# Kernel tuning notes

Hardware: AMD Instinct MI355X
Metric: run time of the kernel (lower is better)

## Reference

```python
import jax, jax.numpy as jnp
import numpy as np

N = 50000
HEADS1, HIM = 8, 16
NEG_SLOPE = 0.2


def gat_conv(x, src, dst, W, a_src, a_dst, bias, heads, out_dim, concat):
    n = x.shape[0]
    h = (x @ W).reshape(n, heads, out_dim)                      # [N,H,D]
    al_src = jnp.einsum('nhd,hd->nh', h, a_src)                  # [N,H]
    al_dst = jnp.einsum('nhd,hd->nh', h, a_dst)                  # [N,H]
    e = jax.nn.leaky_relu(al_src[src] + al_dst[dst], NEG_SLOPE)  # [E,H]
    # segment softmax over incoming edges of each destination node
    e_max = jax.ops.segment_max(e, dst, num_segments=n)
    e_max = jnp.where(jnp.isfinite(e_max), e_max, 0.0)
    ex = jnp.exp(e - e_max[dst])
    denom = jax.ops.segment_sum(ex, dst, num_segments=n)
    denom = jnp.where(denom == 0.0, 1.0, denom)
    alpha = ex / denom[dst]                                      # [E,H]
    msg = h[src] * alpha[:, :, None]                             # [E,H,D]
    out = jax.ops.segment_sum(msg, dst, num_segments=n)          # [N,H,D]
    out = out.reshape(n, heads * out_dim) if concat else out.mean(axis=1)
    return out + bias


def setup_inputs() -> dict:
    key = jax.random.key(0)
    ks = jax.random.split(key, 12)
    num_feature, out_feature, him = 128, 121, HIM
    E = 800000
    x = jax.random.normal(ks[0], (N, num_feature), dtype=jnp.float32)
    edge_index = jax.random.randint(ks[1], (2, E), 0, N, dtype=jnp.int64)
    s = 0.1
    W1 = jax.random.normal(ks[2], (num_feature, HEADS1 * him), dtype=jnp.float32) * s
    a_src1 = jax.random.normal(ks[3], (HEADS1, him), dtype=jnp.float32) * s
    a_dst1 = jax.random.normal(ks[4], (HEADS1, him), dtype=jnp.float32) * s
    b1 = jnp.zeros((HEADS1 * him,), dtype=jnp.float32)
    W2 = jax.random.normal(ks[5], (HEADS1 * him, out_feature), dtype=jnp.float32) * s
    a_src2 = jax.random.normal(ks[6], (1, out_feature), dtype=jnp.float32) * s
    a_dst2 = jax.random.normal(ks[7], (1, out_feature), dtype=jnp.float32) * s
    b2 = jnp.zeros((out_feature,), dtype=jnp.float32)
    return {"x": x, "edge_index": edge_index, "W1": W1, "a_src1": a_src1,
            "a_dst1": a_dst1, "b1": b1, "W2": W2, "a_src2": a_src2,
            "a_dst2": a_dst2, "b2": b2}


def reference(x, edge_index, W1, a_src1, a_dst1, b1, W2, a_src2, a_dst2, b2):
    n = x.shape[0]
    loops = jnp.arange(n, dtype=edge_index.dtype)
    src = jnp.concatenate([edge_index[0], loops])  # add self-loops (PyG default)
    dst = jnp.concatenate([edge_index[1], loops])
    h = gat_conv(x, src, dst, W1, a_src1, a_dst1, b1, HEADS1, HIM, True)
    h = jax.nn.relu(h)
    out = gat_conv(h, src, dst, W2, a_src2, a_dst2, b2, 1, W2.shape[1], True)
    return out
```

## Files before the change

### kernel.cpp

```cpp
#include <hip/hip_runtime.h>
#include <hip/hip_fp16.h>

#define NEG_SLOPE 0.2f

typedef __fp16 half8v __attribute__((ext_vector_type(8)));
typedef float f32x4 __attribute__((ext_vector_type(4)));
typedef unsigned uint4u __attribute__((ext_vector_type(4), aligned(4)));
typedef float f32x4u __attribute__((ext_vector_type(4), aligned(4)));

__device__ __forceinline__ float lrelu(float x) {
    return fmaxf(x, 0.0f) + NEG_SLOPE * fminf(x, 0.0f);
}

__device__ __forceinline__ unsigned fkey(float f) {
    unsigned u = __float_as_uint(f);
    return (u & 0x80000000u) ? ~u : (u | 0x80000000u);
}
__device__ __forceinline__ float funkey(unsigned k) {
    return __uint_as_float((k & 0x80000000u) ? (k & 0x7fffffffu) : ~k);
}


__global__ void pack_kernel(const int* __restrict__ src, const int* __restrict__ dst,
                            unsigned* __restrict__ kv, int E) {
    int e = blockIdx.x * 256 + threadIdx.x;
    if (e < E) kv[e] = ((unsigned)dst[e] << 16) | (unsigned)src[e];
}


__global__ __launch_bounds__(256) void scan_reduce(const int* __restrict__ cnt,
                                                   int* __restrict__ bsum, int n) {
    __shared__ int sm[256];
    int base = blockIdx.x * 1024 + threadIdx.x * 4;
    int s = 0;
#pragma unroll
    for (int j = 0; j < 4; ++j) {
        int i = base + j;
        if (i < n) s += cnt[i];
    }
    sm[threadIdx.x] = s;
    __syncthreads();
#pragma unroll
    for (int off = 128; off >= 1; off >>= 1) {
        if (threadIdx.x < off) sm[threadIdx.x] += sm[threadIdx.x + off];
        __syncthreads();
    }
    if (threadIdx.x == 0) bsum[blockIdx.x] = sm[0];
}

__global__ __launch_bounds__(64) void scan_bsum(int* __restrict__ bsum, int nb) {
    int v = (threadIdx.x < (unsigned)nb) ? bsum[threadIdx.x] : 0;
    int x = v;
#pragma unroll
    for (int off = 1; off < 64; off <<= 1) {
        int y = __shfl_up(x, off);
        if ((int)threadIdx.x >= off) x += y;
    }
    if (threadIdx.x < (unsigned)nb) bsum[threadIdx.x] = x - v;
}

__global__ __launch_bounds__(256) void scan_write(const int* __restrict__ cnt,
                                                  const int* __restrict__ bsum,
                                                  int* __restrict__ rp, int n) {
    __shared__ int sm[256];
    int base = blockIdx.x * 1024 + threadIdx.x * 4;
    int v[4];
    int s = 0;
#pragma unroll
    for (int j = 0; j < 4; ++j) {
        int i = base + j;
        v[j] = (i < n) ? cnt[i] : 0;
        s += v[j];
    }
    sm[threadIdx.x] = s;
    __syncthreads();
#pragma unroll
    for (int off = 1; off < 256; off <<= 1) {
        int y = (threadIdx.x >= off) ? sm[threadIdx.x - off] : 0;
        __syncthreads();
        sm[threadIdx.x] += y;
        __syncthreads();
    }
    int run = sm[threadIdx.x] - s + bsum[blockIdx.x];
#pragma unroll
    for (int j = 0; j < 4; ++j) {
        int i = base + j;
        if (i < n) {
            rp[i] = run;
            run += v[j];
            if (i == n - 1) rp[n] = run;
        }
    }
}


template <int SH>
__global__ __launch_bounds__(256) void rhist_kernel(const unsigned* __restrict__ kv,
                                                    int* __restrict__ h, int E, int nblk) {
    __shared__ int lh[256];
    lh[threadIdx.x] = 0;
    __syncthreads();
    int base = blockIdx.x * 4096;
#pragma unroll
    for (int j = 0; j < 16; ++j) {
        int i = base + j * 256 + threadIdx.x;
        if (i < E) atomicAdd(&lh[(kv[i] >> SH) & 255], 1);
    }
    __syncthreads();
    h[threadIdx.x * nblk + blockIdx.x] = lh[threadIdx.x];
}


template <int SH>
__global__ __launch_bounds__(256) void rscat_kernel(const unsigned* __restrict__ in,
                                                    unsigned* __restrict__ outv,
                                                    const int* __restrict__ scanned,
                                                    int E, int nblk) {
    __shared__ unsigned items[4096];
    __shared__ unsigned sorted[4096];
    __shared__ int lh[256], lstart[256], rbase[256];
    __shared__ int wcnt[4][256];

    int tid = threadIdx.x, blk = blockIdx.x;
    int base = blk * 4096;
    int k = min(4096, E - base);
    lh[tid] = 0;
    rbase[tid] = 0;
#pragma unroll
    for (int j = 0; j < 16; ++j) {
        int idx = j * 256 + tid;
        items[idx] = (base + idx < E) ? in[base + idx] : 0u;
    }
    __syncthreads();
#pragma unroll
    for (int j = 0; j < 16; ++j) {
        int idx = j * 256 + tid;
        if (idx < k) atomicAdd(&lh[(items[idx] >> SH) & 255], 1);
    }
    __syncthreads();
    int sv = lh[tid];
    lstart[tid] = sv;
    __syncthreads();
    for (int off = 1; off < 256; off <<= 1) {
        int y = (tid >= off) ? lstart[tid - off] : 0;
        __syncthreads();
        lstart[tid] += y;
        __syncthreads();
    }
    int excl = lstart[tid] - sv;
    __syncthreads();
    lstart[tid] = excl;
    __syncthreads();

    int lane = tid & 63, wave = tid >> 6;
    for (int it = 0; it < 16; ++it) {
        int idx = it * 256 + tid;
        unsigned v = items[idx];
        int d = (v >> SH) & 255;
        bool valid = idx < k;
        unsigned long long m = __ballot(valid);
#pragma unroll
        for (int b = 0; b < 8; ++b) {
            unsigned long long bb = __ballot((d >> b) & 1);
            m &= ((d >> b) & 1) ? bb : ~bb;
        }
        int lanerank = __popcll(m & ((1ull << lane) - 1ull));
        int wtot = __popcll(m);
        wcnt[0][tid] = 0; wcnt[1][tid] = 0; wcnt[2][tid] = 0; wcnt[3][tid] = 0;
        __syncthreads();
        if (valid && lanerank == 0) wcnt[wave][d] = wtot;
        __syncthreads();
        if (valid) {
            int cw = 0;
            for (int w = 0; w < wave; ++w) cw += wcnt[w][d];
            sorted[lstart[d] + rbase[d] + cw + lanerank] = v;
        }
        __syncthreads();
        rbase[tid] += wcnt[0][tid] + wcnt[1][tid] + wcnt[2][tid] + wcnt[3][tid];
        __syncthreads();
    }
#pragma unroll
    for (int j = 0; j < 16; ++j) {
        int i = j * 256 + tid;
        if (i < k) {
            unsigned v = sorted[i];
            int d = (v >> SH) & 255;
            outv[scanned[d * nblk + blk] + (i - lstart[d])] = v;
        }
    }
}


__global__ void rp_kernel(const unsigned* __restrict__ kv, int* __restrict__ rp,
                          int E, int N) {
    int i = blockIdx.x * 256 + threadIdx.x;
    if (i >= E) return;
    int cur = (int)(kv[i] >> 16);
    int prev = (i == 0) ? -1 : (int)(kv[i - 1] >> 16);
    for (int t = prev + 1; t <= cur; ++t) rp[t] = i;
    if (i == E - 1)
        for (int t = cur + 1; t <= N; ++t) rp[t] = E;
}


template <int H>
__global__ __launch_bounds__(256) void gmax_kernel(const float* __restrict__ a,
                                                   unsigned* __restrict__ gm, int total) {
    __shared__ unsigned sm[256];
    unsigned loc = 0;
    int stride = 256 * gridDim.x;
    for (int i = blockIdx.x * 256 + threadIdx.x; i < total; i += stride)
        loc = max(loc, fkey(a[i]));
    sm[threadIdx.x] = loc;
    __syncthreads();
    for (int off = 128; off >= H; off >>= 1) {
        if (threadIdx.x < off) sm[threadIdx.x] = max(sm[threadIdx.x], sm[threadIdx.x + off]);
        __syncthreads();
    }
    if (threadIdx.x < H) atomicMax(&gm[threadIdx.x], sm[threadIdx.x]);
}


__global__ __launch_bounds__(256) void w1_kernel(const unsigned* __restrict__ kv,
                                                 const float* __restrict__ alS,
                                                 const float* __restrict__ alD,
                                                 const unsigned* __restrict__ gm,
                                                 float* __restrict__ w1t, int E) {
    int e = blockIdx.x * 256 + threadIdx.x;
    if (e >= E) return;
    unsigned k = kv[e];
    int s = (int)(k & 0xFFFFu), t = (int)(k >> 16);
    float sv[8], dv[8];
    *(f32x4*)&sv[0] = *(const f32x4*)(alS + (size_t)s * 8);
    *(f32x4*)&sv[4] = *(const f32x4*)(alS + (size_t)s * 8 + 4);
    *(f32x4*)&dv[0] = *(const f32x4*)(alD + (size_t)t * 8);
    *(f32x4*)&dv[4] = *(const f32x4*)(alD + (size_t)t * 8 + 4);
#pragma unroll
    for (int h = 0; h < 8; ++h) {
        float m = lrelu(funkey(gm[h]) + dv[h]);
        w1t[(size_t)h * E + e] = __expf(lrelu(sv[h] + dv[h]) - m);
    }
}


__global__ void w2_kernel(const unsigned* __restrict__ kv, const float* __restrict__ alS,
                          const float* __restrict__ alD, const unsigned* __restrict__ gm,
                          float* __restrict__ w2v, int E) {
    int e = blockIdx.x * 256 + threadIdx.x;
    if (e >= E) return;
    unsigned k = kv[e];
    int s = (int)(k & 0xFFFFu), t = (int)(k >> 16);
    float adT = alD[t];
    w2v[e] = __expf(lrelu(alS[s] + adT) - lrelu(funkey(gm[0]) + adT));
}


template <int NC, typename AT>
__global__ __launch_bounds__(256) void gemm_mfma(const AT* __restrict__ A,
                                                 const float* __restrict__ B,
                                                 __half* __restrict__ C, int M) {
    __shared__ __half Bt[128][136];

    {
        int t = threadIdx.x;
        int c = t & 127;
        int kq = t >> 7;
#pragma unroll
        for (int ch = 0; ch < 8; ++ch) {
            int k0 = kq * 64 + ch * 8;
            half8v hv;
#pragma unroll
            for (int j = 0; j < 8; ++j) {
                float v = (c < NC) ? B[(size_t)(k0 + j) * NC + c] : 0.0f;
                hv[j] = (__fp16)v;
            }
            *(half8v*)&Bt[c][k0] = hv;
        }
    }
    __syncthreads();

    const int wid = threadIdx.x >> 6;
    const int lane = threadIdx.x & 63;
    const int li = lane & 15;
    const int lg = lane >> 4;

    int row = blockIdx.x * 64 + wid * 16 + li;
    int rowc = min(row, M - 1);

    half8v a[4];
#pragma unroll
    for (int ks = 0; ks < 4; ++ks) {
        int q = ks * 4 + lg;
        if constexpr (sizeof(AT) == 2) {
            a[ks] = *((const half8v*)(A + (size_t)rowc * 128) + q);
        } else {
            const float4* p = (const float4*)(A + (size_t)rowc * 128) + 2 * q;
            float4 a0 = p[0], a1 = p[1];
            half8v hv;
            hv[0] = (__fp16)a0.x; hv[1] = (__fp16)a0.y; hv[2] = (__fp16)a0.z; hv[3] = (__fp16)a0.w;
            hv[4] = (__fp16)a1.x; hv[5] = (__fp16)a1.y; hv[6] = (__fp16)a1.z; hv[7] = (__fp16)a1.w;
            a[ks] = hv;
        }
    }

    f32x4 acc[8];
#pragma unroll
    for (int ct = 0; ct < 8; ++ct) acc[ct] = (f32x4)0.0f;

#pragma unroll
    for (int ks = 0; ks < 4; ++ks) {
#pragma unroll
        for (int ct = 0; ct < 8; ++ct) {
            half8v b = *(const half8v*)&Bt[ct * 16 + li][ks * 32 + 8 * lg];
            acc[ct] = __builtin_amdgcn_mfma_f32_16x16x32_f16(a[ks], b, acc[ct], 0, 0, 0);
        }
    }

    int orow = blockIdx.x * 64 + wid * 16 + 4 * lg;
#pragma unroll
    for (int ct = 0; ct < 8; ++ct) {
#pragma unroll
        for (int r = 0; r < 4; ++r) {
            int rr = orow + r;
            if (rr < M) C[(size_t)rr * 128 + ct * 16 + li] = __float2half(acc[ct][r]);
        }
    }
}


__global__ void al1_kernel(const __half* __restrict__ h1h, const float* __restrict__ as,
                           const float* __restrict__ ad, float* __restrict__ alS,
                           float* __restrict__ alD, int N) {
    int g = blockIdx.x * 256 + threadIdx.x;
    if (g >= N * 8) return;
    int r = g >> 3, h = g & 7;
    const __half2* hp = (const __half2*)(h1h + (size_t)r * 128 + h * 16);
    const float* sp = as + h * 16;
    const float* dp = ad + h * 16;
    float s = 0.f, d = 0.f;
#pragma unroll
    for (int q = 0; q < 8; ++q) {
        float2 v = __half22float2(hp[q]);
        s = fmaf(v.x, sp[2 * q], s);
        d = fmaf(v.x, dp[2 * q], d);
        s = fmaf(v.y, sp[2 * q + 1], s);
        d = fmaf(v.y, dp[2 * q + 1], d);
    }
    alS[g] = s;
    alD[g] = d;
}

__global__ __launch_bounds__(256) void al2_kernel(const __half* __restrict__ h3h,
                                                  const float* __restrict__ as,
                                                  const float* __restrict__ ad,
                                                  float* __restrict__ alS,
                                                  float* __restrict__ alD, int N, int NC) {
    int lane = threadIdx.x & 63;
    int r = blockIdx.x * 4 + (threadIdx.x >> 6);
    if (r >= N) return;
    float s = 0.f, d = 0.f;
    for (int c = lane; c < NC; c += 64) {
        float v = __half2float(h3h[(size_t)r * 128 + c]);
        s = fmaf(v, as[c], s);
        d = fmaf(v, ad[c], d);
    }
#pragma unroll
    for (int off = 32; off; off >>= 1) {
        s += __shfl_down(s, off);
        d += __shfl_down(d, off);
    }
    if (lane == 0) { alS[r] = s; alD[r] = d; }
}


__global__ __launch_bounds__(256) void agg1_kernel(
    const __half* __restrict__ h1h, const float* __restrict__ alS,
    const float* __restrict__ alD, const float* __restrict__ b1,
    const int* __restrict__ rp, const unsigned* __restrict__ kv,
    const float* __restrict__ w1t, const unsigned* __restrict__ gm,
    __half* __restrict__ h2h, int N, int E) {
    int t = blockIdx.x * 4 + (threadIdx.x >> 6);
    if (t >= N) return;
    int lane = threadIdx.x & 63;
    int h = lane >> 3;

    float adh = alD[t * 8 + h];
    float mh = lrelu(funkey(gm[h]) + adh);
    int e0 = rp[t], e1 = rp[t + 1];

    float ex = __expf(lrelu(alS[t * 8 + h] + adh) - mh);
    float dsum = ex, dsum2 = 0.f;
    float2 hs = __half22float2(*(const __half2*)(h1h + (size_t)t * 128 + 2 * lane));
    float fx = ex * hs.x, fy = ex * hs.y;
    const float* wrow = w1t + (size_t)h * E;

    int e = e0;
    for (; e + 8 <= e1; e += 8) {
        uint4u ka = *(const uint4u*)&kv[e];
        uint4u kb = *(const uint4u*)&kv[e + 4];
        f32x4u wa = *(const f32x4u*)&wrow[e];
        f32x4u wb = *(const f32x4u*)&wrow[e + 4];
        float2 f0 = __half22float2(*(const __half2*)(h1h + (size_t)(ka.x & 0xFFFFu) * 128 + 2 * lane));
        float2 f1 = __half22float2(*(const __half2*)(h1h + (size_t)(ka.y & 0xFFFFu) * 128 + 2 * lane));
        float2 f2 = __half22float2(*(const __half2*)(h1h + (size_t)(ka.z & 0xFFFFu) * 128 + 2 * lane));
        float2 f3 = __half22float2(*(const __half2*)(h1h + (size_t)(ka.w & 0xFFFFu) * 128 + 2 * lane));
        float2 f4 = __half22float2(*(const __half2*)(h1h + (size_t)(kb.x & 0xFFFFu) * 128 + 2 * lane));
        float2 f5 = __half22float2(*(const __half2*)(h1h + (size_t)(kb.y & 0xFFFFu) * 128 + 2 * lane));
        float2 f6 = __half22float2(*(const __half2*)(h1h + (size_t)(kb.z & 0xFFFFu) * 128 + 2 * lane));
        float2 f7 = __half22float2(*(const __half2*)(h1h + (size_t)(kb.w & 0xFFFFu) * 128 + 2 * lane));
        dsum += (wa[0] + wa[1]) + (wa[2] + wa[3]);
        dsum2 += (wb[0] + wb[1]) + (wb[2] + wb[3]);
        fx = fmaf(wa[0], f0.x, fx); fy = fmaf(wa[0], f0.y, fy);
        fx = fmaf(wa[1], f1.x, fx); fy = fmaf(wa[1], f1.y, fy);
        fx = fmaf(wa[2], f2.x, fx); fy = fmaf(wa[2], f2.y, fy);
        fx = fmaf(wa[3], f3.x, fx); fy = fmaf(wa[3], f3.y, fy);
        fx = fmaf(wb[0], f4.x, fx); fy = fmaf(wb[0], f4.y, fy);
        fx = fmaf(wb[1], f5.x, fx); fy = fmaf(wb[1], f5.y, fy);
        fx = fmaf(wb[2], f6.x, fx); fy = fmaf(wb[2], f6.y, fy);
        fx = fmaf(wb[3], f7.x, fx); fy = fmaf(wb[3], f7.y, fy);
    }
    if (e + 4 <= e1) {
        uint4u ka = *(const uint4u*)&kv[e];
        f32x4u wa = *(const f32x4u*)&wrow[e];
        float2 f0 = __half22float2(*(const __half2*)(h1h + (size_t)(ka.x & 0xFFFFu) * 128 + 2 * lane));
        float2 f1 = __half22float2(*(const __half2*)(h1h + (size_t)(ka.y & 0xFFFFu) * 128 + 2 * lane));
        float2 f2 = __half22float2(*(const __half2*)(h1h + (size_t)(ka.z & 0xFFFFu) * 128 + 2 * lane));
        float2 f3 = __half22float2(*(const __half2*)(h1h + (size_t)(ka.w & 0xFFFFu) * 128 + 2 * lane));
        dsum += (wa[0] + wa[1]) + (wa[2] + wa[3]);
        fx = fmaf(wa[0], f0.x, fx); fy = fmaf(wa[0], f0.y, fy);
        fx = fmaf(wa[1], f1.x, fx); fy = fmaf(wa[1], f1.y, fy);
        fx = fmaf(wa[2], f2.x, fx); fy = fmaf(wa[2], f2.y, fy);
        fx = fmaf(wa[3], f3.x, fx); fy = fmaf(wa[3], f3.y, fy);
        e += 4;
    }
    for (; e < e1; ++e) {
        int s0 = (int)(kv[e] & 0xFFFFu);
        float w0 = wrow[e];
        float2 f0 = __half22float2(*(const __half2*)(h1h + (size_t)s0 * 128 + 2 * lane));
        dsum2 += w0;
        fx = fmaf(w0, f0.x, fx); fy = fmaf(w0, f0.y, fy);
    }
    dsum += dsum2;
    float inv = 1.0f / dsum;
    float2 bb = *(const float2*)(b1 + 2 * lane);
    float ox = fmaxf(fmaf(fx, inv, bb.x), 0.0f);
    float oy = fmaxf(fmaf(fy, inv, bb.y), 0.0f);
    *(__half2*)(h2h + (size_t)t * 128 + 2 * lane) = __floats2half2_rn(ox, oy);
}


__global__ __launch_bounds__(256) void agg2_kernel(
    const __half* __restrict__ h3h, const float* __restrict__ alS,
    const float* __restrict__ alD, const float* __restrict__ b2,
    const int* __restrict__ rp, const unsigned* __restrict__ kv,
    const float* __restrict__ w2v, const unsigned* __restrict__ gm,
    float* __restrict__ out, int N, int NC) {
    int t = blockIdx.x * 4 + (threadIdx.x >> 6);
    if (t >= N) return;
    int lane = threadIdx.x & 63;

    float adT = alD[t];
    float m = lrelu(funkey(gm[0]) + adT);
    int e0 = rp[t], e1 = rp[t + 1];

    float ex = __expf(lrelu(alS[t] + adT) - m);
    float dsum = ex, dsum2 = 0.f;
    float2 hs = __half22float2(*(const __half2*)(h3h + (size_t)t * 128 + 2 * lane));
    float fx = ex * hs.x, fy = ex * hs.y;

    int e = e0;
    for (; e + 8 <= e1; e += 8) {
        uint4u ka = *(const uint4u*)&kv[e];
        uint4u kb = *(const uint4u*)&kv[e + 4];
        f32x4u wa = *(const f32x4u*)&w2v[e];
        f32x4u wb = *(const f32x4u*)&w2v[e + 4];
        float2 f0 = __half22float2(*(const __half2*)(h3h + (size_t)(ka.x & 0xFFFFu) * 128 + 2 * lane));
        float2 f1 = __half22float2(*(const __half2*)(h3h + (size_t)(ka.y & 0xFFFFu) * 128 + 2 * lane));
        float2 f2 = __half22float2(*(const __half2*)(h3h + (size_t)(ka.z & 0xFFFFu) * 128 + 2 * lane));
        float2 f3 = __half22float2(*(const __half2*)(h3h + (size_t)(ka.w & 0xFFFFu) * 128 + 2 * lane));
        float2 f4 = __half22float2(*(const __half2*)(h3h + (size_t)(kb.x & 0xFFFFu) * 128 + 2 * lane));
        float2 f5 = __half22float2(*(const __half2*)(h3h + (size_t)(kb.y & 0xFFFFu) * 128 + 2 * lane));
        float2 f6 = __half22float2(*(const __half2*)(h3h + (size_t)(kb.z & 0xFFFFu) * 128 + 2 * lane));
        float2 f7 = __half22float2(*(const __half2*)(h3h + (size_t)(kb.w & 0xFFFFu) * 128 + 2 * lane));
        dsum += (wa[0] + wa[1]) + (wa[2] + wa[3]);
        dsum2 += (wb[0] + wb[1]) + (wb[2] + wb[3]);
        fx = fmaf(wa[0], f0.x, fx); fy = fmaf(wa[0], f0.y, fy);
        fx = fmaf(wa[1], f1.x, fx); fy = fmaf(wa[1], f1.y, fy);
        fx = fmaf(wa[2], f2.x, fx); fy = fmaf(wa[2], f2.y, fy);
        fx = fmaf(wa[3], f3.x, fx); fy = fmaf(wa[3], f3.y, fy);
        fx = fmaf(wb[0], f4.x, fx); fy = fmaf(wb[0], f4.y, fy);
        fx = fmaf(wb[1], f5.x, fx); fy = fmaf(wb[1], f5.y, fy);
        fx = fmaf(wb[2], f6.x, fx); fy = fmaf(wb[2], f6.y, fy);
        fx = fmaf(wb[3], f7.x, fx); fy = fmaf(wb[3], f7.y, fy);
    }
    if (e + 4 <= e1) {
        uint4u ka = *(const uint4u*)&kv[e];
        f32x4u wa = *(const f32x4u*)&w2v[e];
        float2 f0 = __half22float2(*(const __half2*)(h3h + (size_t)(ka.x & 0xFFFFu) * 128 + 2 * lane));
        float2 f1 = __half22float2(*(const __half2*)(h3h + (size_t)(ka.y & 0xFFFFu) * 128 + 2 * lane));
        float2 f2 = __half22float2(*(const __half2*)(h3h + (size_t)(ka.z & 0xFFFFu) * 128 + 2 * lane));
        float2 f3 = __half22float2(*(const __half2*)(h3h + (size_t)(ka.w & 0xFFFFu) * 128 + 2 * lane));
        dsum += (wa[0] + wa[1]) + (wa[2] + wa[3]);
        fx = fmaf(wa[0], f0.x, fx); fy = fmaf(wa[0], f0.y, fy);
        fx = fmaf(wa[1], f1.x, fx); fy = fmaf(wa[1], f1.y, fy);
        fx = fmaf(wa[2], f2.x, fx); fy = fmaf(wa[2], f2.y, fy);
        fx = fmaf(wa[3], f3.x, fx); fy = fmaf(wa[3], f3.y, fy);
        e += 4;
    }
    for (; e < e1; ++e) {
        int s0 = (int)(kv[e] & 0xFFFFu);
        float w0 = w2v[e];
        float2 f0 = __half22float2(*(const __half2*)(h3h + (size_t)s0 * 128 + 2 * lane));
        dsum2 += w0;
        fx = fmaf(w0, f0.x, fx); fy = fmaf(w0, f0.y, fy);
    }
    dsum += dsum2;
    float inv = 1.0f / dsum;
    int c0 = 2 * lane, c1 = 2 * lane + 1;
    if (c0 < NC) out[(size_t)t * NC + c0] = fmaf(fx, inv, b2[c0]);
    if (c1 < NC) out[(size_t)t * NC + c1] = fmaf(fy, inv, b2[c1]);
}


extern "C" void kernel_launch(void* const* d_in, const int* in_sizes, int n_in,
                              void* d_out, int out_size, void* d_ws, size_t ws_size,
                              hipStream_t stream) {
    const float* x   = (const float*)d_in[0];
    const int*   ei  = (const int*)d_in[1];
    const float* W1  = (const float*)d_in[2];
    const float* aS1 = (const float*)d_in[3];
    const float* aD1 = (const float*)d_in[4];
    const float* b1  = (const float*)d_in[5];
    const float* W2  = (const float*)d_in[6];
    const float* aS2 = (const float*)d_in[7];
    const float* aD2 = (const float*)d_in[8];
    const float* b2  = (const float*)d_in[9];
    float* out = (float*)d_out;

    const int N = in_sizes[0] / 128;
    const int E = in_sizes[1] / 2;
    const int NC2 = 121;

    const int NBLK = (E + 4095) / 4096;
    const int HN = 256 * NBLK;

    size_t off = 0;
    auto alloc = [&](size_t bytes) {
        size_t o = off;
        off = (off + bytes + 255) & ~(size_t)255;
        return o;
    };
    char* ws = (char*)d_ws;
    unsigned* kv0  = (unsigned*)(ws + alloc((size_t)E * 4));
    unsigned* kv1  = (unsigned*)(ws + alloc((size_t)E * 4));
    int*      h    = (int*)(ws + alloc((size_t)(HN + 1) * 4));
    int*      hs   = (int*)(ws + alloc((size_t)(HN + 1) * 4));
    int*      rp   = (int*)(ws + alloc((size_t)(N + 1) * 4));
    int*      bsum = (int*)(ws + alloc(64 * 4));
    float*    alS1 = (float*)(ws + alloc((size_t)N * 8 * 4));
    float*    alD1 = (float*)(ws + alloc((size_t)N * 8 * 4));
    float*    alS2 = (float*)(ws + alloc((size_t)N * 4));
    float*    alD2 = (float*)(ws + alloc((size_t)N * 4));
    unsigned* gm1  = (unsigned*)(ws + alloc(8 * 4));
    unsigned* gm2  = (unsigned*)(ws + alloc(4));
    float*    w1t  = (float*)(ws + alloc((size_t)E * 8 * 4));
    __half*   h1h  = (__half*)(ws + alloc((size_t)N * 128 * 2));
    __half*   h2h  = (__half*)(ws + alloc((size_t)N * 128 * 2));
    __half*   h3h  = h1h;
    float*    w2v  = (float*)kv1;
    if (ws_size < off) return;

    const int* src = ei;
    const int* dst = ei + E;

    hipMemsetAsync(gm1, 0, 8 * 4, stream);
    hipMemsetAsync(gm2, 0, 4, stream);

    int eb = (E + 255) / 256;
    int snb = (HN + 1023) / 1024;

    pack_kernel<<<eb, 256, 0, stream>>>(src, dst, kv0, E);
    rhist_kernel<16><<<NBLK, 256, 0, stream>>>(kv0, h, E, NBLK);
    scan_reduce<<<snb, 256, 0, stream>>>(h, bsum, HN);
    scan_bsum<<<1, 64, 0, stream>>>(bsum, snb);
    scan_write<<<snb, 256, 0, stream>>>(h, bsum, hs, HN);
    rscat_kernel<16><<<NBLK, 256, 0, stream>>>(kv0, kv1, hs, E, NBLK);
    rhist_kernel<24><<<NBLK, 256, 0, stream>>>(kv1, h, E, NBLK);
    scan_reduce<<<snb, 256, 0, stream>>>(h, bsum, HN);
    scan_bsum<<<1, 64, 0, stream>>>(bsum, snb);
    scan_write<<<snb, 256, 0, stream>>>(h, bsum, hs, HN);
    rscat_kernel<24><<<NBLK, 256, 0, stream>>>(kv1, kv0, hs, E, NBLK);
    rp_kernel<<<eb, 256, 0, stream>>>(kv0, rp, E, N);

    int gmb = (N + 63) / 64;
    int ab = (N + 3) / 4;
    gemm_mfma<128, float><<<gmb, 256, 0, stream>>>(x, W1, h1h, N);
    al1_kernel<<<(N * 8 + 255) / 256, 256, 0, stream>>>(h1h, aS1, aD1, alS1, alD1, N);
    gmax_kernel<8><<<128, 256, 0, stream>>>(alS1, gm1, N * 8);
    w1_kernel<<<eb, 256, 0, stream>>>(kv0, alS1, alD1, gm1, w1t, E);
    agg1_kernel<<<ab, 256, 0, stream>>>(h1h, alS1, alD1, b1, rp, kv0, w1t, gm1, h2h, N, E);

    gemm_mfma<121, __half><<<gmb, 256, 0, stream>>>(h2h, W2, h3h, N);
    al2_kernel<<<ab, 256, 0, stream>>>(h3h, aS2, aD2, alS2, alD2, N, NC2);
    gmax_kernel<1><<<128, 256, 0, stream>>>(alS2, gm2, N);
    w2_kernel<<<eb, 256, 0, stream>>>(kv0, alS2, alD2, gm2, w2v, E);
    agg2_kernel<<<ab, 256, 0, stream>>>(h3h, alS2, alD2, b2, rp, kv0, w2v, gm2, out, N, NC2);
}
```

Baseline: 236.4 us.

## Fuse pack into radix scatter, fold global max into alpha kernels, unroll aggregation

Removes the separate pack kernel by building the dst/src key inside the first radix scatter pass, and removes both gmax kernels by computing the per-head max reduction inside al1/al2. Radix sort blocks shrink from 4096 to 1024 items, which adds more blocks and a 256-wide block-sum scan. Aggregation loops are unrolled to 16 edges per iteration to keep more gathers in flight. The N bound checks in agg kernels are dropped, which relies on N being a multiple of 4; the smaller blocks also raise scan and histogram traffic.

```diff
diff --git a/kernel.cpp b/kernel.cpp
--- a/kernel.cpp
+++ b/kernel.cpp
@@ -18,13 +18,6 @@
 }
 __device__ __forceinline__ float funkey(unsigned k) {
     return __uint_as_float((k & 0x80000000u) ? (k & 0x7fffffffu) : ~k);
-}
-
-
-__global__ void pack_kernel(const int* __restrict__ src, const int* __restrict__ dst,
-                            unsigned* __restrict__ kv, int E) {
-    int e = blockIdx.x * 256 + threadIdx.x;
-    if (e < E) kv[e] = ((unsigned)dst[e] << 16) | (unsigned)src[e];
 }
 
 
@@ -48,15 +41,18 @@
     if (threadIdx.x == 0) bsum[blockIdx.x] = sm[0];
 }
 
-__global__ __launch_bounds__(64) void scan_bsum(int* __restrict__ bsum, int nb) {
+__global__ __launch_bounds__(256) void scan_bsum256(int* __restrict__ bsum, int nb) {
+    __shared__ int sm[256];
     int v = (threadIdx.x < (unsigned)nb) ? bsum[threadIdx.x] : 0;
-    int x = v;
-#pragma unroll
-    for (int off = 1; off < 64; off <<= 1) {
-        int y = __shfl_up(x, off);
-        if ((int)threadIdx.x >= off) x += y;
-    }
-    if (threadIdx.x < (unsigned)nb) bsum[threadIdx.x] = x - v;
+    sm[threadIdx.x] = v;
+    __syncthreads();
+    for (int off = 1; off < 256; off <<= 1) {
+        int y = (threadIdx.x >= off) ? sm[threadIdx.x - off] : 0;
+        __syncthreads();
+        sm[threadIdx.x] += y;
+        __syncthreads();
+    }
+    if (threadIdx.x < (unsigned)nb) bsum[threadIdx.x] = sm[threadIdx.x] - v;
 }
 
 __global__ __launch_bounds__(256) void scan_write(const int* __restrict__ cnt,
@@ -94,46 +90,68 @@
 }
 
 
-template <int SH>
-__global__ __launch_bounds__(256) void rhist_kernel(const unsigned* __restrict__ kv,
-                                                    int* __restrict__ h, int E, int nblk) {
+__global__ __launch_bounds__(256) void rhist1_kernel(const int* __restrict__ dst,
+                                                     int* __restrict__ h, int E, int nblk) {
     __shared__ int lh[256];
     lh[threadIdx.x] = 0;
     __syncthreads();
-    int base = blockIdx.x * 4096;
-#pragma unroll
-    for (int j = 0; j < 16; ++j) {
+    int base = blockIdx.x * 1024;
+#pragma unroll
+    for (int j = 0; j < 4; ++j) {
         int i = base + j * 256 + threadIdx.x;
-        if (i < E) atomicAdd(&lh[(kv[i] >> SH) & 255], 1);
+        if (i < E) atomicAdd(&lh[dst[i] & 255], 1);
     }
     __syncthreads();
     h[threadIdx.x * nblk + blockIdx.x] = lh[threadIdx.x];
 }
 
-
-template <int SH>
+__global__ __launch_bounds__(256) void rhist2_kernel(const unsigned* __restrict__ kv,
+                                                     int* __restrict__ h, int E, int nblk) {
+    __shared__ int lh[256];
+    lh[threadIdx.x] = 0;
+    __syncthreads();
+    int base = blockIdx.x * 1024;
+#pragma unroll
+    for (int j = 0; j < 4; ++j) {
+        int i = base + j * 256 + threadIdx.x;
+        if (i < E) atomicAdd(&lh[kv[i] >> 24], 1);
+    }
+    __syncthreads();
+    h[threadIdx.x * nblk + blockIdx.x] = lh[threadIdx.x];
+}
+
+template <int SH, bool PACK>
 __global__ __launch_bounds__(256) void rscat_kernel(const unsigned* __restrict__ in,
+                                                    const int* __restrict__ srcp,
+                                                    const int* __restrict__ dstp,
                                                     unsigned* __restrict__ outv,
                                                     const int* __restrict__ scanned,
                                                     int E, int nblk) {
-    __shared__ unsigned items[4096];
-    __shared__ unsigned sorted[4096];
+    __shared__ unsigned items[1024];
+    __shared__ unsigned sorted[1024];
     __shared__ int lh[256], lstart[256], rbase[256];
     __shared__ int wcnt[4][256];
 
     int tid = threadIdx.x, blk = blockIdx.x;
-    int base = blk * 4096;
-    int k = min(4096, E - base);
+    int base = blk * 1024;
+    int k = min(1024, E - base);
     lh[tid] = 0;
     rbase[tid] = 0;
 #pragma unroll
-    for (int j = 0; j < 16; ++j) {
+    for (int j = 0; j < 4; ++j) {
         int idx = j * 256 + tid;
-        items[idx] = (base + idx < E) ? in[base + idx] : 0u;
-    }
-    __syncthreads();
-#pragma unroll
-    for (int j = 0; j < 16; ++j) {
+        unsigned v = 0u;
+        if (base + idx < E) {
+            if constexpr (PACK)
+                v = ((unsigned)dstp[base + idx] << 16) | (unsigned)srcp[base + idx];
+            else
+                v = in[base + idx];
+        }
+        items[idx] = v;
+    }
+    __syncthreads();
+#pragma unroll
+    for (int j = 0; j < 4; ++j) {
         int idx = j * 256 + tid;
         if (idx < k) atomicAdd(&lh[(items[idx] >> SH) & 255], 1);
     }
@@ -153,7 +171,8 @@
     __syncthreads();
 
     int lane = tid & 63, wave = tid >> 6;
-    for (int it = 0; it < 16; ++it) {
+#pragma unroll
+    for (int it = 0; it < 4; ++it) {
         int idx = it * 256 + tid;
         unsigned v = items[idx];
         int d = (v >> SH) & 255;
@@ -180,7 +199,7 @@
         __syncthreads();
     }
 #pragma unroll
-    for (int j = 0; j < 16; ++j) {
+    for (int j = 0; j < 4; ++j) {
         int i = j * 256 + tid;
         if (i < k) {
             unsigned v = sorted[i];
@@ -200,24 +219,6 @@
     for (int t = prev + 1; t <= cur; ++t) rp[t] = i;
     if (i == E - 1)
         for (int t = cur + 1; t <= N; ++t) rp[t] = E;
-}
-
-
-template <int H>
-__global__ __launch_bounds__(256) void gmax_kernel(const float* __restrict__ a,
-                                                   unsigned* __restrict__ gm, int total) {
-    __shared__ unsigned sm[256];
-    unsigned loc = 0;
-    int stride = 256 * gridDim.x;
-    for (int i = blockIdx.x * 256 + threadIdx.x; i < total; i += stride)
-        loc = max(loc, fkey(a[i]));
-    sm[threadIdx.x] = loc;
-    __syncthreads();
-    for (int off = 128; off >= H; off >>= 1) {
-        if (threadIdx.x < off) sm[threadIdx.x] = max(sm[threadIdx.x], sm[threadIdx.x + off]);
-        __syncthreads();
-    }
-    if (threadIdx.x < H) atomicMax(&gm[threadIdx.x], sm[threadIdx.x]);
 }
 
 
@@ -242,7 +243,6 @@
     }
 }
 
-
 __global__ void w2_kernel(const unsigned* __restrict__ kv, const float* __restrict__ alS,
                           const float* __restrict__ alD, const unsigned* __restrict__ gm,
                           float* __restrict__ w2v, int E) {
@@ -328,36 +328,52 @@
 }
 
 
-__global__ void al1_kernel(const __half* __restrict__ h1h, const float* __restrict__ as,
-                           const float* __restrict__ ad, float* __restrict__ alS,
-                           float* __restrict__ alD, int N) {
+__global__ __launch_bounds__(256) void al1_kernel(const __half* __restrict__ h1h,
+                                                  const float* __restrict__ as,
+                                                  const float* __restrict__ ad,
+                                                  float* __restrict__ alS,
+                                                  float* __restrict__ alD,
+                                                  unsigned* __restrict__ gm, int N) {
+    __shared__ unsigned sm[256];
     int g = blockIdx.x * 256 + threadIdx.x;
-    if (g >= N * 8) return;
-    int r = g >> 3, h = g & 7;
-    const __half2* hp = (const __half2*)(h1h + (size_t)r * 128 + h * 16);
-    const float* sp = as + h * 16;
-    const float* dp = ad + h * 16;
-    float s = 0.f, d = 0.f;
-#pragma unroll
-    for (int q = 0; q < 8; ++q) {
-        float2 v = __half22float2(hp[q]);
-        s = fmaf(v.x, sp[2 * q], s);
-        d = fmaf(v.x, dp[2 * q], d);
-        s = fmaf(v.y, sp[2 * q + 1], s);
-        d = fmaf(v.y, dp[2 * q + 1], d);
-    }
-    alS[g] = s;
-    alD[g] = d;
+    unsigned loc = 0;
+    if (g < N * 8) {
+        int r = g >> 3, h = g & 7;
+        const __half2* hp = (const __half2*)(h1h + (size_t)r * 128 + h * 16);
+        const float* sp = as + h * 16;
+        const float* dp = ad + h * 16;
+        float s = 0.f, d = 0.f;
+#pragma unroll
+        for (int q = 0; q < 8; ++q) {
+            float2 v = __half22float2(hp[q]);
+            s = fmaf(v.x, sp[2 * q], s);
+            d = fmaf(v.x, dp[2 * q], d);
+            s = fmaf(v.y, sp[2 * q + 1], s);
+            d = fmaf(v.y, dp[2 * q + 1], d);
+        }
+        alS[g] = s;
+        alD[g] = d;
+        loc = fkey(s);
+    }
+    sm[threadIdx.x] = loc;
+    __syncthreads();
+    for (int off = 128; off >= 8; off >>= 1) {
+        if (threadIdx.x < off) sm[threadIdx.x] = max(sm[threadIdx.x], sm[threadIdx.x + off]);
+        __syncthreads();
+    }
+    if (threadIdx.x < 8) atomicMax(&gm[threadIdx.x], sm[threadIdx.x]);
 }
 
 __global__ __launch_bounds__(256) void al2_kernel(const __half* __restrict__ h3h,
                                                   const float* __restrict__ as,
                                                   const float* __restrict__ ad,
                                                   float* __restrict__ alS,
-                                                  float* __restrict__ alD, int N, int NC) {
+                                                  float* __restrict__ alD,
+                                                  unsigned* __restrict__ gm, int N, int NC) {
+    __shared__ unsigned sm4[4];
     int lane = threadIdx.x & 63;
-    int r = blockIdx.x * 4 + (threadIdx.x >> 6);
-    if (r >= N) return;
+    int wid = threadIdx.x >> 6;
+    int r = blockIdx.x * 4 + wid;
     float s = 0.f, d = 0.f;
     for (int c = lane; c < NC; c += 64) {
         float v = __half2float(h3h[(size_t)r * 128 + c]);
@@ -369,7 +385,16 @@
         s += __shfl_down(s, off);
         d += __shfl_down(d, off);
     }
-    if (lane == 0) { alS[r] = s; alD[r] = d; }
+    if (lane == 0) {
+        alS[r] = s;
+        alD[r] = d;
+        sm4[wid] = fkey(s);
+    }
+    __syncthreads();
+    if (threadIdx.x == 0) {
+        unsigned m = max(max(sm4[0], sm4[1]), max(sm4[2], sm4[3]));
+        atomicMax(&gm[0], m);
+    }
 }
 
 
@@ -380,7 +405,6 @@
     const float* __restrict__ w1t, const unsigned* __restrict__ gm,
     __half* __restrict__ h2h, int N, int E) {
     int t = blockIdx.x * 4 + (threadIdx.x >> 6);
-    if (t >= N) return;
     int lane = threadIdx.x & 63;
     int h = lane >> 3;
 
@@ -395,7 +419,35 @@
     const float* wrow = w1t + (size_t)h * E;
 
     int e = e0;
-    for (; e + 8 <= e1; e += 8) {
+    for (; e + 16 <= e1; e += 16) {
+        uint4u kk[4];
+        f32x4u ww[4];
+#pragma unroll
+        for (int q = 0; q < 4; ++q) {
+            kk[q] = *(const uint4u*)&kv[e + 4 * q];
+            ww[q] = *(const f32x4u*)&wrow[e + 4 * q];
+        }
+        float2 ff[16];
+#pragma unroll
+        for (int q = 0; q < 4; ++q)
+#pragma unroll
+            for (int r = 0; r < 4; ++r)
+                ff[q * 4 + r] = __half22float2(
+                    *(const __half2*)(h1h + (size_t)(kk[q][r] & 0xFFFFu) * 128 + 2 * lane));
+#pragma unroll
+        for (int q = 0; q < 4; ++q) {
+            if (q & 1) dsum2 += (ww[q][0] + ww[q][1]) + (ww[q][2] + ww[q][3]);
+            else       dsum  += (ww[q][0] + ww[q][1]) + (ww[q][2] + ww[q][3]);
+#pragma unroll
+            for (int r = 0; r < 4; ++r) {
+                float w = ww[q][r];
+                float2 f = ff[q * 4 + r];
+                fx = fmaf(w, f.x, fx);
+                fy = fmaf(w, f.y, fy);
+            }
+        }
+    }
+    if (e + 8 <= e1) {
         uint4u ka = *(const uint4u*)&kv[e];
         uint4u kb = *(const uint4u*)&kv[e + 4];
         f32x4u wa = *(const f32x4u*)&wrow[e];
@@ -418,6 +470,7 @@
         fx = fmaf(wb[1], f5.x, fx); fy = fmaf(wb[1], f5.y, fy);
         fx = fmaf(wb[2], f6.x, fx); fy = fmaf(wb[2], f6.y, fy);
         fx = fmaf(wb[3], f7.x, fx); fy = fmaf(wb[3], f7.y, fy);
+        e += 8;
     }
     if (e + 4 <= e1) {
         uint4u ka = *(const uint4u*)&kv[e];
@@ -456,7 +509,6 @@
     const float* __restrict__ w2v, const unsigned* __restrict__ gm,
     float* __restrict__ out, int N, int NC) {
     int t = blockIdx.x * 4 + (threadIdx.x >> 6);
-    if (t >= N) return;
     int lane = threadIdx.x & 63;
 
     float adT = alD[t];
@@ -469,7 +521,35 @@
     float fx = ex * hs.x, fy = ex * hs.y;
 
     int e = e0;
-    for (; e + 8 <= e1; e += 8) {
+    for (; e + 16 <= e1; e += 16) {
+        uint4u kk[4];
+        f32x4u ww[4];
+#pragma unroll
+        for (int q = 0; q < 4; ++q) {
+            kk[q] = *(const uint4u*)&kv[e + 4 * q];
+            ww[q] = *(const f32x4u*)&w2v[e + 4 * q];
+        }
+        float2 ff[16];
+#pragma unroll
+        for (int q = 0; q < 4; ++q)
+#pragma unroll
+            for (int r = 0; r < 4; ++r)
+                ff[q * 4 + r] = __half22float2(
+                    *(const __half2*)(h3h + (size_t)(kk[q][r] & 0xFFFFu) * 128 + 2 * lane));
+#pragma unroll
+        for (int q = 0; q < 4; ++q) {
+            if (q & 1) dsum2 += (ww[q][0] + ww[q][1]) + (ww[q][2] + ww[q][3]);
+            else       dsum  += (ww[q][0] + ww[q][1]) + (ww[q][2] + ww[q][3]);
+#pragma unroll
+            for (int r = 0; r < 4; ++r) {
+                float w = ww[q][r];
+                float2 f = ff[q * 4 + r];
+                fx = fmaf(w, f.x, fx);
+                fy = fmaf(w, f.y, fy);
+            }
+        }
+    }
+    if (e + 8 <= e1) {
         uint4u ka = *(const uint4u*)&kv[e];
         uint4u kb = *(const uint4u*)&kv[e + 4];
         f32x4u wa = *(const f32x4u*)&w2v[e];
@@ -492,6 +572,7 @@
         fx = fmaf(wb[1], f5.x, fx); fy = fmaf(wb[1], f5.y, fy);
         fx = fmaf(wb[2], f6.x, fx); fy = fmaf(wb[2], f6.y, fy);
         fx = fmaf(wb[3], f7.x, fx); fy = fmaf(wb[3], f7.y, fy);
+        e += 8;
     }
     if (e + 4 <= e1) {
         uint4u ka = *(const uint4u*)&kv[e];
@@ -541,7 +622,7 @@
     const int E = in_sizes[1] / 2;
     const int NC2 = 121;
 
-    const int NBLK = (E + 4095) / 4096;
+    const int NBLK = (E + 1023) / 1024;
     const int HN = 256 * NBLK;
 
     size_t off = 0;
@@ -556,7 +637,7 @@
     int*      h    = (int*)(ws + alloc((size_t)(HN + 1) * 4));
     int*      hs   = (int*)(ws + alloc((size_t)(HN + 1) * 4));
     int*      rp   = (int*)(ws + alloc((size_t)(N + 1) * 4));
-    int*      bsum = (int*)(ws + alloc(64 * 4));
+    int*      bsum = (int*)(ws + alloc(256 * 4));
     float*    alS1 = (float*)(ws + alloc((size_t)N * 8 * 4));
     float*    alD1 = (float*)(ws + alloc((size_t)N * 8 * 4));
     float*    alS2 = (float*)(ws + alloc((size_t)N * 4));
@@ -579,30 +660,27 @@
     int eb = (E + 255) / 256;
     int snb = (HN + 1023) / 1024;
 
-    pack_kernel<<<eb, 256, 0, stream>>>(src, dst, kv0, E);
-    rhist_kernel<16><<<NBLK, 256, 0, stream>>>(kv0, h, E, NBLK);
+    rhist1_kernel<<<NBLK, 256, 0, stream>>>(dst, h, E, NBLK);
     scan_reduce<<<snb, 256, 0, stream>>>(h, bsum, HN);
-    scan_bsum<<<1, 64, 0, stream>>>(bsum, snb);
+    scan_bsum256<<<1, 256, 0, stream>>>(bsum, snb);
     scan_write<<<snb, 256, 0, stream>>>(h, bsum, hs, HN);
-    rscat_kernel<16><<<NBLK, 256, 0, stream>>>(kv0, kv1, hs, E, NBLK);
-    rhist_kernel<24><<<NBLK, 256, 0, stream>>>(kv1, h, E, NBLK);
+    rscat_kernel<16, true><<<NBLK, 256, 0, stream>>>(nullptr, src, dst, kv1, hs, E, NBLK);
+    rhist2_kernel<<<NBLK, 256, 0, stream>>>(kv1, h, E, NBLK);
     scan_reduce<<<snb, 256, 0, stream>>>(h, bsum, HN);
-    scan_bsum<<<1, 64, 0, stream>>>(bsum, snb);
+    scan_bsum256<<<1, 256, 0, stream>>>(bsum, snb);
     scan_write<<<snb, 256, 0, stream>>>(h, bsum, hs, HN);
-    rscat_kernel<24><<<NBLK, 256, 0, stream>>>(kv1, kv0, hs, E, NBLK);
+    rscat_kernel<24, false><<<NBLK, 256, 0, stream>>>(kv1, nullptr, nullptr, kv0, hs, E, NBLK);
     rp_kernel<<<eb, 256, 0, stream>>>(kv0, rp, E, N);
 
     int gmb = (N + 63) / 64;
     int ab = (N + 3) / 4;
     gemm_mfma<128, float><<<gmb, 256, 0, stream>>>(x, W1, h1h, N);
-    al1_kernel<<<(N * 8 + 255) / 256, 256, 0, stream>>>(h1h, aS1, aD1, alS1, alD1, N);
-    gmax_kernel<8><<<128, 256, 0, stream>>>(alS1, gm1, N * 8);
+    al1_kernel<<<(N * 8 + 255) / 256, 256, 0, stream>>>(h1h, aS1, aD1, alS1, alD1, gm1, N);
     w1_kernel<<<eb, 256, 0, stream>>>(kv0, alS1, alD1, gm1, w1t, E);
     agg1_kernel<<<ab, 256, 0, stream>>>(h1h, alS1, alD1, b1, rp, kv0, w1t, gm1, h2h, N, E);
 
     gemm_mfma<121, __half><<<gmb, 256, 0, stream>>>(h2h, W2, h3h, N);
-    al2_kernel<<<ab, 256, 0, stream>>>(h3h, aS2, aD2, alS2, alD2, N, NC2);
-    gmax_kernel<1><<<128, 256, 0, stream>>>(alS2, gm2, N);
+    al2_kernel<<<ab, 256, 0, stream>>>(h3h, aS2, aD2, alS2, alD2, gm2, N, NC2);
     w2_kernel<<<eb, 256, 0, stream>>>(kv0, alS2, alD2, gm2, w2v, E);
     agg2_kernel<<<ab, 256, 0, stream>>>(h3h, alS2, alD2, b2, rp, kv0, w2v, gm2, out, N, NC2);
 }
```

Result: slower. 352.0 us (+48.9%).
